# Optimization experiments

Hardware: AMD Instinct MI355X
Metric: run time of the kernel (lower is better)

Reference implementation:

```python
import jax, jax.numpy as jnp
import numpy as np

PC_RANGE = np.array([-15.0, -30.0, -2.0, 15.0, 30.0, 2.0], dtype=np.float32)
POST_CENTER_RANGE = jnp.array([-20.0, -35.0, -20.0, -35.0, 20.0, 35.0, 20.0, 35.0], dtype=jnp.float32)
MAX_NUM = 100
NUM_CLASSES = 3


def setup_inputs() -> dict:
    key = jax.random.key(0)
    k1, k2, k3 = jax.random.split(key, 3)
    L, B, Q, C, P = 6, 128, 2000, 3, 20
    return {
        "all_cls_scores": jax.random.normal(k1, (L, B, Q, C), dtype=jnp.float32),
        "all_bbox_preds": jax.random.uniform(k2, (L, B, Q, 4), dtype=jnp.float32),
        "all_pts_preds": jax.random.uniform(k3, (L, B, Q, P, 2), dtype=jnp.float32),
    }


def _decode(cls_scores, bbox_preds, pts_preds):
    # cls_scores [B,Q,C], bbox_preds [B,Q,4] (cx,cy,w,h normalized), pts_preds [B,Q,P,2]
    B = cls_scores.shape[0]
    flat = jax.nn.sigmoid(cls_scores).reshape(B, -1)          # [B, Q*C]
    scores, idx = jax.lax.top_k(flat, MAX_NUM)                # [B, M]
    labels = idx % NUM_CLASSES
    bbox_index = idx // NUM_CLASSES
    bbox_s = jnp.take_along_axis(bbox_preds, bbox_index[:, :, None], axis=1)          # [B,M,4]
    pts_s = jnp.take_along_axis(pts_preds, bbox_index[:, :, None, None], axis=1)      # [B,M,P,2]

    # box_center_to_corner: (cx,cy,w,h) -> (x1,y1,x2,y2)
    cx, cy, w, h = jnp.split(bbox_s, 4, axis=-1)
    corners = jnp.concatenate([cx - 0.5 * w, cy - 0.5 * h, cx + 0.5 * w, cy + 0.5 * h], axis=-1)

    sx = PC_RANGE[3] - PC_RANGE[0]
    sy = PC_RANGE[4] - PC_RANGE[1]
    scale = jnp.array([sx, sy, sx, sy], dtype=jnp.float32)
    offset = jnp.array([PC_RANGE[0], PC_RANGE[1], PC_RANGE[0], PC_RANGE[1]], dtype=jnp.float32)
    boxes = corners * scale + offset                           # [B,M,4]

    pts_d = jnp.stack([pts_s[..., 0] * sx + PC_RANGE[0],
                       pts_s[..., 1] * sy + PC_RANGE[1]], axis=-1)  # [B,M,P,2]

    mask = jnp.all(boxes >= POST_CENTER_RANGE[:4], axis=-1) & \
           jnp.all(boxes <= POST_CENTER_RANGE[4:], axis=-1)    # [B,M]
    return boxes, scores, labels, pts_d, mask


def reference(all_cls_scores, all_bbox_preds, all_pts_preds):
    # Only the last decoder layer is decoded, as in MapTRNMSFreeCoder.decode
    boxes, scores, labels, pts, mask = _decode(
        all_cls_scores[-1], all_bbox_preds[-1], all_pts_preds[-1]
    )
    # Torch filters by boolean mask (ragged); here we pad: zero-out masked-off
    # entries and return the mask so downstream can recover the ragged result.
    boxes = jnp.where(mask[..., None], boxes, 0.0)
    scores = jnp.where(mask, scores, 0.0)
    labels = jnp.where(mask, labels, -1)
    pts = jnp.where(mask[..., None, None], pts, 0.0)
    return boxes, scores, labels, pts, mask
```

## Files before the change

### kernel.cpp

```cpp
#include <hip/hip_runtime.h>
#include <math.h>

#define LAYERS 6
#define BATCH 128
#define NQ 2000
#define NC 3
#define NP 20
#define TOPK 100
#define QC (NQ * NC)
#define NTHREADS 256
#define TIE_CAP 256

#define BOXES_OFF 0
#define SCORES_OFF 51200
#define LABELS_OFF 64000
#define PTS_OFF 76800
#define MASK_OFF 588800

__global__ __launch_bounds__(NTHREADS) void maptr_post_kernel(
    const float* __restrict__ cls,
    const float* __restrict__ bbox,
    const float* __restrict__ pts,
    float* __restrict__ out)
{
    const int b = blockIdx.x;
    const int tid = threadIdx.x;

    __shared__ unsigned int su[QC];
    __shared__ int hist[256];
    __shared__ int scanb[256];
    __shared__ unsigned int cand_u[TOPK];
    __shared__ int cand_i[TOPK];
    __shared__ int tie_i[TIE_CAP];
    __shared__ int sT, sGt, nCand, nTie;
    __shared__ float topv[TOPK];
    __shared__ int topi[TOPK];
    __shared__ int sbi[TOPK];
    __shared__ float smask[TOPK];

    if (tid == 0) { nCand = 0; nTie = 0; }

    const float* clsb = cls + (size_t)b * QC;
    for (int i = tid; i < QC; i += NTHREADS) {
        unsigned int bits = __float_as_uint(clsb[i]);
        su[i] = (bits & 0x80000000u) ? ~bits : (bits | 0x80000000u);
    }
    __syncthreads();

    unsigned int prefix = 0, pmask = 0;
    int need = TOPK;
    #pragma unroll
    for (int pass = 0; pass < 4; ++pass) {
        const int shift = 24 - 8 * pass;
        hist[tid] = 0;
        __syncthreads();
        for (int i = tid; i < QC; i += NTHREADS) {
            unsigned int u = su[i];
            if ((u & pmask) == prefix)
                atomicAdd(&hist[(u >> shift) & 0xffu], 1);
        }
        __syncthreads();
        scanb[tid] = hist[tid];
        __syncthreads();
        #pragma unroll
        for (int off = 1; off < 256; off <<= 1) {
            int add = (tid + off < 256) ? scanb[tid + off] : 0;
            __syncthreads();
            scanb[tid] += add;
            __syncthreads();
        }
        if (scanb[tid] >= need && (tid == 255 || scanb[tid + 1] < need)) {
            sT = tid;
            sGt = (tid == 255) ? 0 : scanb[tid + 1];
        }
        __syncthreads();
        prefix |= ((unsigned int)sT) << shift;
        pmask |= 0xffu << shift;
        need -= sGt;
        __syncthreads();
    }
    const unsigned int T32 = prefix;
    const int R = need;

    for (int i = tid; i < QC; i += NTHREADS) {
        unsigned int u = su[i];
        if (u > T32) {
            int p = atomicAdd(&nCand, 1);
            cand_u[p] = u; cand_i[p] = i;
        } else if (u == T32) {
            int p = atomicAdd(&nTie, 1);
            if (p < TIE_CAP) tie_i[p] = i;
        }
    }
    __syncthreads();
    const int G = nCand;
    const int E = (nTie < TIE_CAP) ? nTie : TIE_CAP;
    if (tid < E) {
        int mine = tie_i[tid];
        int rk = 0;
        for (int j = 0; j < E; ++j) rk += (tie_i[j] < mine);
        if (rk < R) { cand_u[G + rk] = T32; cand_i[G + rk] = mine; }
    }
    __syncthreads();

    if (tid < TOPK) {
        unsigned int u = cand_u[tid];
        int ii = cand_i[tid];
        int rank = 0;
        for (int j = 0; j < TOPK; ++j) {
            unsigned int uj = cand_u[j];
            int ij = cand_i[j];
            rank += (uj > u) || (uj == u && ij < ii);
        }
        unsigned int bits = (u & 0x80000000u) ? (u & 0x7fffffffu) : ~u;
        topv[rank] = __uint_as_float(bits);
        topi[rank] = ii;
    }
    __syncthreads();

    float* const boxes_out = out + BOXES_OFF;
    float* const scores_out = out + SCORES_OFF;
    float* const labels_out = out + LABELS_OFF;
    float* const pts_out = out + PTS_OFF;
    float* const mask_out = out + MASK_OFF;

    if (tid < TOPK) {
        const int m = tid;
        const int idx = topi[m];
        const float lv = topv[m];
        const float score = 1.0f / (1.0f + expf(-lv));
        const int bi = idx / 3;
        const int label = idx - bi * 3;

        const float4 bb = *(const float4*)(bbox + ((size_t)b * NQ + bi) * 4);
        const float bx1 = (bb.x - 0.5f * bb.z) * 30.0f - 15.0f;
        const float by1 = (bb.y - 0.5f * bb.w) * 60.0f - 30.0f;
        const float bx2 = (bb.x + 0.5f * bb.z) * 30.0f - 15.0f;
        const float by2 = (bb.y + 0.5f * bb.w) * 60.0f - 30.0f;

        const bool mk = (bx1 >= -20.0f) && (by1 >= -35.0f) && (bx2 >= -20.0f) && (by2 >= -35.0f) &&
                        (bx1 <= 20.0f) && (by1 <= 35.0f) && (bx2 <= 20.0f) && (by2 <= 35.0f);

        const size_t bm = (size_t)b * TOPK + m;
        boxes_out[bm * 4 + 0] = mk ? bx1 : 0.0f;
        boxes_out[bm * 4 + 1] = mk ? by1 : 0.0f;
        boxes_out[bm * 4 + 2] = mk ? bx2 : 0.0f;
        boxes_out[bm * 4 + 3] = mk ? by2 : 0.0f;
        scores_out[bm] = mk ? score : 0.0f;
        labels_out[bm] = mk ? (float)label : -1.0f;
        mask_out[bm] = mk ? 1.0f : 0.0f;
        sbi[m] = bi;
        smask[m] = mk ? 1.0f : 0.0f;
    }
    __syncthreads();

    for (int t = tid; t < TOPK * NP; t += NTHREADS) {
        const int m = t / NP;
        const int p = t - m * NP;
        const int bi = sbi[m];
        const bool mk = smask[m] != 0.0f;
        const float2 pv = *(const float2*)(pts + (((size_t)b * NQ + bi) * NP + p) * 2);
        const size_t o = (((size_t)b * TOPK + m) * NP + p) * 2;
        pts_out[o + 0] = mk ? (pv.x * 30.0f - 15.0f) : 0.0f;
        pts_out[o + 1] = mk ? (pv.y * 60.0f - 30.0f) : 0.0f;
    }
}

extern "C" void kernel_launch(void* const* d_in, const int* in_sizes, int n_in,
                              void* d_out, int out_size, void* d_ws, size_t ws_size,
                              hipStream_t stream) {
    const float* cls = (const float*)d_in[0] + (size_t)(LAYERS - 1) * BATCH * NQ * NC;
    const float* bbox = (const float*)d_in[1] + (size_t)(LAYERS - 1) * BATCH * NQ * 4;
    const float* pts = (const float*)d_in[2] + (size_t)(LAYERS - 1) * BATCH * NQ * NP * 2;
    maptr_post_kernel<<<BATCH, NTHREADS, 0, stream>>>(cls, bbox, pts, (float*)d_out);
}
```

Before: 313.2 us.

## Use 3-pass 11-bit radix select with register-held keys and wave-shuffle scan

Replaces the 4-pass 8-bit radix select over shared memory with 3 passes of 11/11/10 bits. The converted keys are now held in a per-thread register array instead of a shared buffer. The 256-entry log-step scan, which needed a barrier at every step, becomes a per-thread serial sum plus a wave shuffle reduction and cross-wave totals. The goal is fewer block barriers and passes, and less histogram atomic contention. In exchange it uses larger 2048-bin histograms, and the runtime-bounded loop over the register array could push it into scratch memory.

Measured after the change: 317.8 us. About the same (+1.5%).

```diff
diff --git a/kernel.cpp b/kernel.cpp
--- a/kernel.cpp
+++ b/kernel.cpp
@@ -9,6 +9,8 @@
 #define TOPK 100
 #define QC (NQ * NC)
 #define NTHREADS 256
+#define MAXPER 24
+#define REM 112
 #define TIE_CAP 256
 
 #define BOXES_OFF 0
@@ -16,6 +18,63 @@
 #define LABELS_OFF 64000
 #define PTS_OFF 76800
 #define MASK_OFF 588800
+
+template <int SHIFT, int NBITS>
+__device__ inline void radix_pass(const unsigned int* __restrict__ rv, int cnt,
+                                  unsigned int& prefix, unsigned int& pmask, int& need,
+                                  int* hist, int* scanb, int* wtot,
+                                  int* sBin, int* sGt,
+                                  int tid, int lane, int wid)
+{
+    constexpr int NB = 1 << NBITS;
+    constexpr unsigned int DMASK = (unsigned int)(NB - 1);
+    constexpr int BP = NB / NTHREADS;
+
+    #pragma unroll
+    for (int j = 0; j < BP; ++j) hist[tid * BP + j] = 0;
+    __syncthreads();
+
+    for (int k = 0; k < cnt; ++k) {
+        const unsigned int u = rv[k];
+        if ((u & pmask) == prefix) atomicAdd(&hist[(u >> SHIFT) & DMASK], 1);
+    }
+    __syncthreads();
+
+    int v[BP];
+    int tot = 0;
+    #pragma unroll
+    for (int j = BP - 1; j >= 0; --j) { tot += hist[tid * BP + j]; v[j] = tot; }
+
+    int incl = tot;
+    #pragma unroll
+    for (int off = 1; off < 64; off <<= 1) {
+        const int o = __shfl_down(incl, off);
+        incl += (lane + off < 64) ? o : 0;
+    }
+    if (lane == 0) wtot[wid] = incl;
+    __syncthreads();
+
+    int higher = 0;
+    for (int w = wid + 1; w < 4; ++w) higher += wtot[w];
+    const int base = higher + (incl - tot);
+
+    #pragma unroll
+    for (int j = 0; j < BP; ++j) scanb[tid * BP + j] = base + v[j];
+    __syncthreads();
+
+    #pragma unroll
+    for (int j = 0; j < BP; ++j) {
+        const int bin = tid * BP + j;
+        const int s = base + v[j];
+        const int nxt = (bin == NB - 1) ? 0 : scanb[bin + 1];
+        if (s >= need && (bin == NB - 1 || nxt < need)) { *sBin = bin; *sGt = nxt; }
+    }
+    __syncthreads();
+
+    prefix |= ((unsigned int)*sBin) << SHIFT;
+    pmask |= DMASK << SHIFT;
+    need -= *sGt;
+}
 
 __global__ __launch_bounds__(NTHREADS) void maptr_post_kernel(
     const float* __restrict__ cls,
@@ -25,14 +84,17 @@
 {
     const int b = blockIdx.x;
     const int tid = threadIdx.x;
-
-    __shared__ unsigned int su[QC];
-    __shared__ int hist[256];
-    __shared__ int scanb[256];
+    const int lane = tid & 63;
+    const int wid = tid >> 6;
+
+    __shared__ int hist[2048];
+    __shared__ int scanb[2048];
+    __shared__ int wtot[4];
+    __shared__ int sBin, sGt;
     __shared__ unsigned int cand_u[TOPK];
     __shared__ int cand_i[TOPK];
     __shared__ int tie_i[TIE_CAP];
-    __shared__ int sT, sGt, nCand, nTie;
+    __shared__ int nCand, nTie;
     __shared__ float topv[TOPK];
     __shared__ int topi[TOPK];
     __shared__ int sbi[TOPK];
@@ -41,54 +103,30 @@
     if (tid == 0) { nCand = 0; nTie = 0; }
 
     const float* clsb = cls + (size_t)b * QC;
-    for (int i = tid; i < QC; i += NTHREADS) {
-        unsigned int bits = __float_as_uint(clsb[i]);
-        su[i] = (bits & 0x80000000u) ? ~bits : (bits | 0x80000000u);
-    }
-    __syncthreads();
+    const int cnt = (tid < REM) ? MAXPER : (MAXPER - 1);
+    unsigned int rv[MAXPER];
+    for (int k = 0; k < cnt; ++k) {
+        const unsigned int bits = __float_as_uint(clsb[tid + k * NTHREADS]);
+        rv[k] = (bits & 0x80000000u) ? ~bits : (bits | 0x80000000u);
+    }
 
     unsigned int prefix = 0, pmask = 0;
     int need = TOPK;
-    #pragma unroll
-    for (int pass = 0; pass < 4; ++pass) {
-        const int shift = 24 - 8 * pass;
-        hist[tid] = 0;
-        __syncthreads();
-        for (int i = tid; i < QC; i += NTHREADS) {
-            unsigned int u = su[i];
-            if ((u & pmask) == prefix)
-                atomicAdd(&hist[(u >> shift) & 0xffu], 1);
-        }
-        __syncthreads();
-        scanb[tid] = hist[tid];
-        __syncthreads();
-        #pragma unroll
-        for (int off = 1; off < 256; off <<= 1) {
-            int add = (tid + off < 256) ? scanb[tid + off] : 0;
-            __syncthreads();
-            scanb[tid] += add;
-            __syncthreads();
-        }
-        if (scanb[tid] >= need && (tid == 255 || scanb[tid + 1] < need)) {
-            sT = tid;
-            sGt = (tid == 255) ? 0 : scanb[tid + 1];
-        }
-        __syncthreads();
-        prefix |= ((unsigned int)sT) << shift;
-        pmask |= 0xffu << shift;
-        need -= sGt;
-        __syncthreads();
-    }
+    radix_pass<21, 11>(rv, cnt, prefix, pmask, need, hist, scanb, wtot, &sBin, &sGt, tid, lane, wid);
+    radix_pass<10, 11>(rv, cnt, prefix, pmask, need, hist, scanb, wtot, &sBin, &sGt, tid, lane, wid);
+    radix_pass<0, 10>(rv, cnt, prefix, pmask, need, hist, scanb, wtot, &sBin, &sGt, tid, lane, wid);
+
     const unsigned int T32 = prefix;
     const int R = need;
 
-    for (int i = tid; i < QC; i += NTHREADS) {
-        unsigned int u = su[i];
+    for (int k = 0; k < cnt; ++k) {
+        const unsigned int u = rv[k];
+        const int i = tid + k * NTHREADS;
         if (u > T32) {
-            int p = atomicAdd(&nCand, 1);
+            const int p = atomicAdd(&nCand, 1);
             cand_u[p] = u; cand_i[p] = i;
         } else if (u == T32) {
-            int p = atomicAdd(&nTie, 1);
+            const int p = atomicAdd(&nTie, 1);
             if (p < TIE_CAP) tie_i[p] = i;
         }
     }
@@ -96,7 +134,7 @@
     const int G = nCand;
     const int E = (nTie < TIE_CAP) ? nTie : TIE_CAP;
     if (tid < E) {
-        int mine = tie_i[tid];
+        const int mine = tie_i[tid];
         int rk = 0;
         for (int j = 0; j < E; ++j) rk += (tie_i[j] < mine);
         if (rk < R) { cand_u[G + rk] = T32; cand_i[G + rk] = mine; }
@@ -104,15 +142,15 @@
     __syncthreads();
 
     if (tid < TOPK) {
-        unsigned int u = cand_u[tid];
-        int ii = cand_i[tid];
+        const unsigned int u = cand_u[tid];
+        const int ii = cand_i[tid];
         int rank = 0;
         for (int j = 0; j < TOPK; ++j) {
-            unsigned int uj = cand_u[j];
-            int ij = cand_i[j];
+            const unsigned int uj = cand_u[j];
+            const int ij = cand_i[j];
             rank += (uj > u) || (uj == u && ij < ii);
         }
-        unsigned int bits = (u & 0x80000000u) ? (u & 0x7fffffffu) : ~u;
+        const unsigned int bits = (u & 0x80000000u) ? (u & 0x7fffffffu) : ~u;
         topv[rank] = __uint_as_float(bits);
         topi[rank] = ii;
     }
```
